# Performance work log

Hardware: AMD Instinct MI355X
Metric: run time of the kernel (lower is better)

## Reference

```python
import jax, jax.numpy as jnp
import numpy as np

GRID = 32
N_NODES = GRID * GRID          # 1024
PATCH = 1
C_IN = 3
NODE_F = C_IN * PATCH * PATCH  # 3
HID = 256
N_CLASSES = 10


def _build_norm_adj():
    # 5-point grid stencil + self loops, symmetrically normalized: D^-1/2 A D^-1/2
    adj = np.zeros((N_NODES, N_NODES), dtype=np.float32)
    idx = np.arange(N_NODES)
    i, j = idx // GRID, idx % GRID
    adj[idx, idx] = 1.0
    for di, dj in [(-1, 0), (1, 0), (0, -1), (0, 1)]:
        ni, nj = i + di, j + dj
        ok = (ni >= 0) & (ni < GRID) & (nj >= 0) & (nj < GRID)
        adj[idx[ok], (ni * GRID + nj)[ok]] = 1.0
    deg = adj.sum(axis=1)
    dis = np.where(deg > 0, deg ** -0.5, 0.0).astype(np.float32)
    return jnp.asarray(dis[:, None] * adj * dis[None, :])


def _image_to_graph(x):
    # [B,C,H,W] -> [B, grid, patch, grid, patch] blocks -> [B, N, C*patch^2]
    B = x.shape[0]
    x = x.reshape(B, C_IN, GRID, PATCH, GRID, PATCH)
    x = jnp.transpose(x, (0, 2, 4, 1, 3, 5))
    return x.reshape(B, N_NODES, NODE_F)


def setup_inputs() -> dict:
    key = jax.random.key(0)
    ks = jax.random.split(key, 10)
    s = 0.05
    return {
        "x": jax.random.normal(ks[0], (256, 3, 32, 32), dtype=jnp.float32),
        "W1": jax.random.normal(ks[1], (HID, NODE_F), dtype=jnp.float32) * s,
        "b1": jnp.zeros((HID,), dtype=jnp.float32),
        "W2": jax.random.normal(ks[2], (HID, HID), dtype=jnp.float32) * s,
        "b2": jnp.zeros((HID,), dtype=jnp.float32),
        "W3": jax.random.normal(ks[3], (HID // 2, HID), dtype=jnp.float32) * s,
        "b3": jnp.zeros((HID // 2,), dtype=jnp.float32),
        "Wc": jax.random.normal(ks[4], (N_CLASSES, N_NODES * (HID // 2)), dtype=jnp.float32) * s,
        "bc": jnp.zeros((N_CLASSES,), dtype=jnp.float32),
        "adj": _build_norm_adj(),
    }


def _gc(h, W, b, adj):
    # Linear, then fixed-adjacency aggregation, then ReLU
    h = jnp.einsum('bnf,hf->bnh', h, W) + b
    h = jnp.einsum('mn,bnh->bmh', adj, h)
    return jax.nn.relu(h)


def reference(x, W1, b1, W2, b2, W3, b3, Wc, bc, adj):
    h = _image_to_graph(x)                 # [B, N, 3]
    h = _gc(h, W1, b1, adj)                # [B, N, 256]
    h = _gc(h, W2, b2, adj)                # [B, N, 256]
    h = _gc(h, W3, b3, adj)                # [B, N, 128]
    h = h.reshape(h.shape[0], -1)          # [B, N*128]
    return h @ Wc.T + bc                   # [B, 10]
```

## Files before the change

kernel.cpp:

```cpp
#include <hip/hip_runtime.h>
#include <stdint.h>

#define N_NODES 1024
#define NCLS 10
#define KDIM 131072

typedef unsigned short u16;
typedef __bf16 bf16x8 __attribute__((ext_vector_type(8)));
typedef float f32x4 __attribute__((ext_vector_type(4)));

__device__ __forceinline__ float b2f(u16 u) {
  union { float f; uint32_t u; } v; v.u = ((uint32_t)u) << 16; return v.f;
}
__device__ __forceinline__ float b2f_lo(uint32_t u) {
  union { float f; uint32_t u; } v; v.u = u << 16; return v.f;
}
__device__ __forceinline__ float b2f_hi(uint32_t u) {
  union { float f; uint32_t u; } v; v.u = u & 0xFFFF0000u; return v.f;
}
__device__ __forceinline__ u16 f2b(float f) {
  union { float f; uint32_t u; } v; v.f = f;
  uint32_t r = v.u + 0x7FFF + ((v.u >> 16) & 1);
  return (u16)(r >> 16);
}
__device__ __forceinline__ uint32_t pack2(float a, float b) {
  return (uint32_t)f2b(a) | ((uint32_t)f2b(b) << 16);
}

__device__ __forceinline__ void async_copy16(const u16* g, u16* l) {
  __builtin_amdgcn_global_load_lds(
      (const __attribute__((address_space(1))) void*)g,
      (__attribute__((address_space(3))) void*)l, 16, 0, 0);
}

__global__ __launch_bounds__(256) void cvt_w_kernel(const float* __restrict__ w,
                                                    u16* __restrict__ o, int n) {
  int i = blockIdx.x * 256 + threadIdx.x;
  if (i < n) o[i] = f2b(w[i]);
}

__global__ __launch_bounds__(256) void prep_wc_kernel(const float* __restrict__ wc,
                                                      u16* __restrict__ o) {
  int i = blockIdx.x * 256 + threadIdx.x;
  int row = i >> 17;
  int col = i & (KDIM - 1);
  o[i] = (row < NCLS) ? f2b(wc[row * KDIM + col]) : (u16)0;
}

__global__ __launch_bounds__(256) void prep_tab_kernel(const float* __restrict__ adj,
                                                       int* __restrict__ nbi,
                                                       float* __restrict__ nbc,
                                                       float* __restrict__ r) {
  int m = blockIdx.x * 256 + threadIdx.x;
  if (m >= N_NODES) return;
  int i = m >> 5, j = m & 31;
  const float* arow = adj + (size_t)m * N_NODES;
  int n[5]; float c[5];
  n[0] = m;                      c[0] = arow[m];
  n[1] = (i > 0)  ? m - 32 : m;  c[1] = (i > 0)  ? arow[m - 32] : 0.f;
  n[2] = (i < 31) ? m + 32 : m;  c[2] = (i < 31) ? arow[m + 32] : 0.f;
  n[3] = (j > 0)  ? m - 1  : m;  c[3] = (j > 0)  ? arow[m - 1]  : 0.f;
  n[4] = (j < 31) ? m + 1  : m;  c[4] = (j < 31) ? arow[m + 1]  : 0.f;
  float s = 0.f;
#pragma unroll
  for (int t = 0; t < 5; t++) { nbi[m * 5 + t] = n[t]; nbc[m * 5 + t] = c[t]; s += c[t]; }
  r[m] = s;
}

__global__ __launch_bounds__(256) void outinit_kernel(const float* __restrict__ bc,
                                                      float* __restrict__ out) {
  int idx = blockIdx.x * 256 + threadIdx.x;
  if (idx < 256 * NCLS) out[idx] = bc[idx % NCLS];
}

__global__ __launch_bounds__(256) void l1agg_kernel(
    const float* __restrict__ x,
    const float* __restrict__ W1,
    const float* __restrict__ b1,
    const int* __restrict__ nbi, const float* __restrict__ nbc,
    const float* __restrict__ r,
    u16* __restrict__ g)
{
  __shared__ u16 h1s[128 * 256];
  __shared__ float gxs[128][4];
  __shared__ float W1s[768];
  __shared__ float b1s[256];
  int p0 = blockIdx.x * 64;
  int b = p0 >> 10;
  int m0 = p0 & 1023;
  int e0 = m0 - 32;
  int tid = threadIdx.x;

  b1s[tid] = b1[tid];
  for (int i = tid; i < 768; i += 256) W1s[i] = W1[i];

  if (tid < 128) {
    int n = e0 + tid;
    float g0 = 0.f, g1 = 0.f, g2 = 0.f, rn = 0.f;
    if (n >= 0 && n < N_NODES) {
      const float* xb = x + (size_t)b * 3072;
#pragma unroll
      for (int t = 0; t < 5; t++) {
        int nb = nbi[n * 5 + t]; float cf = nbc[n * 5 + t];
        g0 += cf * xb[nb];
        g1 += cf * xb[1024 + nb];
        g2 += cf * xb[2048 + nb];
      }
      rn = r[n];
    }
    gxs[tid][0] = g0; gxs[tid][1] = g1; gxs[tid][2] = g2; gxs[tid][3] = rn;
  }
  __syncthreads();

  int ch8 = (tid & 31) * 8;
  float w[8][3], bb[8];
#pragma unroll
  for (int c = 0; c < 8; c++) {
    w[c][0] = W1s[(ch8 + c) * 3];
    w[c][1] = W1s[(ch8 + c) * 3 + 1];
    w[c][2] = W1s[(ch8 + c) * 3 + 2];
    bb[c] = b1s[ch8 + c];
  }

#pragma unroll
  for (int it = 0; it < 16; it++) {
    int node = (tid >> 5) + it * 8;
    float g0 = gxs[node][0], g1 = gxs[node][1], g2 = gxs[node][2], rn = gxs[node][3];
    uint32_t pk[4];
#pragma unroll
    for (int c = 0; c < 8; c += 2) {
      float z0 = fmaxf(g0 * w[c][0] + g1 * w[c][1] + g2 * w[c][2] + rn * bb[c], 0.f);
      float z1 = fmaxf(g0 * w[c+1][0] + g1 * w[c+1][1] + g2 * w[c+1][2] + rn * bb[c+1], 0.f);
      pk[c >> 1] = pack2(z0, z1);
    }
    *(uint4*)&h1s[node * 256 + ch8] = *(uint4*)pk;
  }
  __syncthreads();

#pragma unroll
  for (int it = 0; it < 8; it++) {
    int node = (tid >> 5) + it * 8;
    int m = m0 + node;
    float acc[8] = {};
#pragma unroll
    for (int t = 0; t < 5; t++) {
      int nb = nbi[m * 5 + t]; float cf = nbc[m * 5 + t];
      uint4 v = *(const uint4*)&h1s[(nb - e0) * 256 + ch8];
      acc[0] += cf * b2f_lo(v.x); acc[1] += cf * b2f_hi(v.x);
      acc[2] += cf * b2f_lo(v.y); acc[3] += cf * b2f_hi(v.y);
      acc[4] += cf * b2f_lo(v.z); acc[5] += cf * b2f_hi(v.z);
      acc[6] += cf * b2f_lo(v.w); acc[7] += cf * b2f_hi(v.w);
    }
    uint4 o;
    o.x = pack2(acc[0], acc[1]); o.y = pack2(acc[2], acc[3]);
    o.z = pack2(acc[4], acc[5]); o.w = pack2(acc[6], acc[7]);
    *(uint4*)&g[(size_t)(p0 + node) * 256 + ch8] = o;
  }
}

__global__ __launch_bounds__(256) void agg_kernel(
    const u16* __restrict__ h,
    const int* __restrict__ nbi, const float* __restrict__ nbc,
    u16* __restrict__ g)
{
  int p = (blockIdx.x * 256 + threadIdx.x) >> 5;
  int lane = threadIdx.x & 31;
  int b = p >> 10, m = p & 1023;
  const u16* base = h + ((size_t)b << 10) * 256;
  int col = lane * 8;
  float acc[8] = {};
#pragma unroll
  for (int t = 0; t < 5; t++) {
    int nb = nbi[m * 5 + t]; float cf = nbc[m * 5 + t];
    uint4 v = *(const uint4*)(base + (size_t)nb * 256 + col);
    acc[0] += cf * b2f_lo(v.x); acc[1] += cf * b2f_hi(v.x);
    acc[2] += cf * b2f_lo(v.y); acc[3] += cf * b2f_hi(v.y);
    acc[4] += cf * b2f_lo(v.z); acc[5] += cf * b2f_hi(v.z);
    acc[6] += cf * b2f_lo(v.w); acc[7] += cf * b2f_hi(v.w);
  }
  uint4 o;
  o.x = pack2(acc[0], acc[1]); o.y = pack2(acc[2], acc[3]);
  o.z = pack2(acc[4], acc[5]); o.w = pack2(acc[6], acc[7]);
  *(uint4*)(g + (size_t)p * 256 + col) = o;
}

__global__ __launch_bounds__(256) void mm_kernel(
    const u16* __restrict__ A, const u16* __restrict__ W,
    const float* __restrict__ bias, const float* __restrict__ r,
    u16* __restrict__ C, int N)
{
  const int K = 256;
  __shared__ u16 As[128 * 32];
  __shared__ u16 Bs[128 * 32];
  int m0 = blockIdx.x * 128;
  int n0 = blockIdx.y * 128;
  int tid = threadIdx.x;
  int w = tid >> 6, l = tid & 63;
  int wm = w >> 1, wn = w & 1;

  f32x4 acc[4][4] = {};

  int srow = w * 32 + (l >> 2);
  int skoff = (l & 3) * 8;
  int lrow = l & 15, lq = l >> 4;

  for (int k0 = 0; k0 < K; k0 += 32) {
    const u16* ga = A + (size_t)(m0 + srow) * K + k0 + skoff;
    const u16* gb = W + (size_t)(n0 + srow) * K + k0 + skoff;
    async_copy16(ga,          &As[(w * 32) * 32]);
    async_copy16(ga + 16 * K, &As[(w * 32 + 16) * 32]);
    async_copy16(gb,          &Bs[(w * 32) * 32]);
    async_copy16(gb + 16 * K, &Bs[(w * 32 + 16) * 32]);
    __syncthreads();

    const u16* pa = &As[(wm * 64 + lrow) * 32 + lq * 8];
    const u16* pb = &Bs[(wn * 64 + lrow) * 32 + lq * 8];
    bf16x8 af[4], bf[4];
#pragma unroll
    for (int t = 0; t < 4; t++) {
      af[t] = *(const bf16x8*)(pa + t * 16 * 32);
      bf[t] = *(const bf16x8*)(pb + t * 16 * 32);
    }
#pragma unroll
    for (int mt = 0; mt < 4; mt++)
#pragma unroll
      for (int nt = 0; nt < 4; nt++)
        acc[mt][nt] = __builtin_amdgcn_mfma_f32_16x16x32_bf16(af[mt], bf[nt], acc[mt][nt], 0, 0, 0);
    __syncthreads();
  }

#pragma unroll
  for (int mt = 0; mt < 4; mt++)
#pragma unroll
    for (int nt = 0; nt < 4; nt++) {
      f32x4 v = acc[mt][nt];
      int col = n0 + wn * 64 + nt * 16 + lrow;
      float bs = bias[col];
#pragma unroll
      for (int i2 = 0; i2 < 4; i2++) {
        int row = m0 + wm * 64 + mt * 16 + lq * 4 + i2;
        float val = v[i2] + r[row & 1023] * bs;
        C[(size_t)row * N + col] = f2b(fmaxf(val, 0.f));
      }
    }
}

__global__ __launch_bounds__(256) void cls_kernel(
    const u16* __restrict__ h3,
    const u16* __restrict__ Wcb,
    float* __restrict__ out,
    int b0)
{
  int mt = blockIdx.x;
  int split = blockIdx.y;
  int w = threadIdx.x >> 6, l = threadIdx.x & 63;
  int lrow = l & 15, lq = l >> 4;
  f32x4 acc = {};
  int kbase = split * 4096 + w * 1024;
  const u16* pa = h3 + (size_t)(mt * 16 + lrow) * KDIM + kbase + lq * 8;
  const u16* pb = Wcb + (size_t)lrow * KDIM + kbase + lq * 8;
#pragma unroll 4
  for (int kk = 0; kk < 1024; kk += 32) {
    bf16x8 a = *(const bf16x8*)(pa + kk);
    bf16x8 b = *(const bf16x8*)(pb + kk);
    acc = __builtin_amdgcn_mfma_f32_16x16x32_bf16(a, b, acc, 0, 0, 0);
  }
  if (lrow < NCLS) {
#pragma unroll
    for (int i2 = 0; i2 < 4; i2++) {
      int b = b0 + mt * 16 + lq * 4 + i2;
      atomicAdd(&out[b * NCLS + lrow], acc[i2]);
    }
  }
}

extern "C" void kernel_launch(void* const* d_in, const int* in_sizes, int n_in,
                              void* d_out, int out_size, void* d_ws, size_t ws_size,
                              hipStream_t stream) {
  const float* x   = (const float*)d_in[0];
  const float* W1  = (const float*)d_in[1];
  const float* b1  = (const float*)d_in[2];
  const float* W2  = (const float*)d_in[3];
  const float* b2  = (const float*)d_in[4];
  const float* W3  = (const float*)d_in[5];
  const float* b3  = (const float*)d_in[6];
  const float* Wc  = (const float*)d_in[7];
  const float* bc  = (const float*)d_in[8];
  const float* adj = (const float*)d_in[9];
  float* out = (float*)d_out;
  const int B = 256;

  uint8_t* ws = (uint8_t*)d_ws;
  u16* W2b = (u16*)ws;  ws += (size_t)256 * 256 * 2;
  u16* W3b = (u16*)ws;  ws += (size_t)128 * 256 * 2;
  u16* Wcb = (u16*)ws;  ws += (size_t)16 * KDIM * 2;
  float* rr  = (float*)ws; ws += 1024 * 4;
  int*   nbi = (int*)ws;   ws += 1024 * 5 * 4;
  float* nbc = (float*)ws; ws += 1024 * 5 * 4;
  uintptr_t al = ((uintptr_t)ws + 255) & ~(uintptr_t)255;
  ws = (uint8_t*)al;
  size_t used = (size_t)(ws - (uint8_t*)d_ws);
  size_t avail = (ws_size > used) ? ws_size - used : 0;
  int chunk = 256;
  while (chunk > 32 && (size_t)chunk * 1024 * 256 * 2 * 2 > avail) chunk >>= 1;
  u16* bufA = (u16*)ws;
  u16* bufB = bufA + (size_t)chunk * 1024 * 256;

  cvt_w_kernel<<<256, 256, 0, stream>>>(W2, W2b, 256 * 256);
  cvt_w_kernel<<<128, 256, 0, stream>>>(W3, W3b, 128 * 256);
  prep_wc_kernel<<<(16 * KDIM) / 256, 256, 0, stream>>>(Wc, Wcb);
  prep_tab_kernel<<<4, 256, 0, stream>>>(adj, nbi, nbc, rr);
  outinit_kernel<<<(256 * NCLS + 255) / 256, 256, 0, stream>>>(bc, out);

  for (int b0 = 0; b0 < B; b0 += chunk) {
    const float* xb = x + (size_t)b0 * 3 * 1024;
    int M = chunk * 1024;
    l1agg_kernel<<<M / 64, 256, 0, stream>>>(xb, W1, b1, nbi, nbc, rr, bufB);
    {
      dim3 g(M / 128, 2);
      mm_kernel<<<g, 256, 0, stream>>>(bufB, W2b, b2, rr, bufA, 256);
    }
    agg_kernel<<<M / 8, 256, 0, stream>>>(bufA, nbi, nbc, bufB);
    {
      dim3 g(M / 128, 1);
      mm_kernel<<<g, 256, 0, stream>>>(bufB, W3b, b3, rr, bufA, 128);
    }
    dim3 gc(chunk / 16, 32);
    cls_kernel<<<gc, 256, 0, stream>>>(bufA, Wcb, out, b0);
  }
}
```

Measured before the change: 399.6 us.

## Fuse layer-3 aggregation into GEMM prologue and widen K tile with swizzled LDS

Removes the standalone aggregation kernel for layer 3. The 5-neighbor stencil sum is now computed while loading the A tile into LDS inside a new fused GEMM kernel, which avoids one full write and re-read of the intermediate activation buffer. The GEMM K step grows from 32 to 64 with an XOR-swizzled LDS layout to reduce bank conflicts and halve the number of barriers. The cost is that neighbor rows are gathered with plain synchronous loads in the GEMM prologue, and each block re-reads halo rows, which may stall the MFMA pipeline.

```diff
diff --git a/kernel.cpp b/kernel.cpp
--- a/kernel.cpp
+++ b/kernel.cpp
@@ -158,40 +158,14 @@
   }
 }
 
-__global__ __launch_bounds__(256) void agg_kernel(
-    const u16* __restrict__ h,
-    const int* __restrict__ nbi, const float* __restrict__ nbc,
-    u16* __restrict__ g)
-{
-  int p = (blockIdx.x * 256 + threadIdx.x) >> 5;
-  int lane = threadIdx.x & 31;
-  int b = p >> 10, m = p & 1023;
-  const u16* base = h + ((size_t)b << 10) * 256;
-  int col = lane * 8;
-  float acc[8] = {};
-#pragma unroll
-  for (int t = 0; t < 5; t++) {
-    int nb = nbi[m * 5 + t]; float cf = nbc[m * 5 + t];
-    uint4 v = *(const uint4*)(base + (size_t)nb * 256 + col);
-    acc[0] += cf * b2f_lo(v.x); acc[1] += cf * b2f_hi(v.x);
-    acc[2] += cf * b2f_lo(v.y); acc[3] += cf * b2f_hi(v.y);
-    acc[4] += cf * b2f_lo(v.z); acc[5] += cf * b2f_hi(v.z);
-    acc[6] += cf * b2f_lo(v.w); acc[7] += cf * b2f_hi(v.w);
-  }
-  uint4 o;
-  o.x = pack2(acc[0], acc[1]); o.y = pack2(acc[2], acc[3]);
-  o.z = pack2(acc[4], acc[5]); o.w = pack2(acc[6], acc[7]);
-  *(uint4*)(g + (size_t)p * 256 + col) = o;
-}
-
 __global__ __launch_bounds__(256) void mm_kernel(
     const u16* __restrict__ A, const u16* __restrict__ W,
     const float* __restrict__ bias, const float* __restrict__ r,
     u16* __restrict__ C, int N)
 {
   const int K = 256;
-  __shared__ u16 As[128 * 32];
-  __shared__ u16 Bs[128 * 32];
+  __shared__ u16 As[128 * 64];
+  __shared__ u16 Bs[128 * 64];
   int m0 = blockIdx.x * 128;
   int n0 = blockIdx.y * 128;
   int tid = threadIdx.x;
@@ -200,32 +174,40 @@
 
   f32x4 acc[4][4] = {};
 
-  int srow = w * 32 + (l >> 2);
-  int skoff = (l & 3) * 8;
+  int r8 = l >> 3, oct = l & 7;
+  int so = (oct ^ r8) << 3;
   int lrow = l & 15, lq = l >> 4;
-
-  for (int k0 = 0; k0 < K; k0 += 32) {
-    const u16* ga = A + (size_t)(m0 + srow) * K + k0 + skoff;
-    const u16* gb = W + (size_t)(n0 + srow) * K + k0 + skoff;
-    async_copy16(ga,          &As[(w * 32) * 32]);
-    async_copy16(ga + 16 * K, &As[(w * 32 + 16) * 32]);
-    async_copy16(gb,          &Bs[(w * 32) * 32]);
-    async_copy16(gb + 16 * K, &Bs[(w * 32 + 16) * 32]);
+  int o0 = (lq ^ (lrow & 7)) << 3;
+  int o1 = o0 ^ 32;
+
+  const u16* ga0 = A + (size_t)(m0 + w * 32 + r8) * K + so;
+  const u16* gb0 = W + (size_t)(n0 + w * 32 + r8) * K + so;
+
+  for (int k0 = 0; k0 < K; k0 += 64) {
+#pragma unroll
+    for (int q = 0; q < 4; q++) {
+      async_copy16(ga0 + q * 8 * K + k0, &As[(w * 32 + q * 8) * 64]);
+      async_copy16(gb0 + q * 8 * K + k0, &Bs[(w * 32 + q * 8) * 64]);
+    }
     __syncthreads();
 
-    const u16* pa = &As[(wm * 64 + lrow) * 32 + lq * 8];
-    const u16* pb = &Bs[(wn * 64 + lrow) * 32 + lq * 8];
-    bf16x8 af[4], bf[4];
+    const u16* pa = &As[(wm * 64 + lrow) * 64];
+    const u16* pb = &Bs[(wn * 64 + lrow) * 64];
+    bf16x8 af[4][2], bf[4][2];
 #pragma unroll
     for (int t = 0; t < 4; t++) {
-      af[t] = *(const bf16x8*)(pa + t * 16 * 32);
-      bf[t] = *(const bf16x8*)(pb + t * 16 * 32);
-    }
-#pragma unroll
-    for (int mt = 0; mt < 4; mt++)
-#pragma unroll
-      for (int nt = 0; nt < 4; nt++)
-        acc[mt][nt] = __builtin_amdgcn_mfma_f32_16x16x32_bf16(af[mt], bf[nt], acc[mt][nt], 0, 0, 0);
+      af[t][0] = *(const bf16x8*)(pa + t * 16 * 64 + o0);
+      af[t][1] = *(const bf16x8*)(pa + t * 16 * 64 + o1);
+      bf[t][0] = *(const bf16x8*)(pb + t * 16 * 64 + o0);
+      bf[t][1] = *(const bf16x8*)(pb + t * 16 * 64 + o1);
+    }
+#pragma unroll
+    for (int kh = 0; kh < 2; kh++)
+#pragma unroll
+      for (int mt = 0; mt < 4; mt++)
+#pragma unroll
+        for (int nt = 0; nt < 4; nt++)
+          acc[mt][nt] = __builtin_amdgcn_mfma_f32_16x16x32_bf16(af[mt][kh], bf[nt][kh], acc[mt][nt], 0, 0, 0);
     __syncthreads();
   }
 
@@ -235,6 +217,114 @@
     for (int nt = 0; nt < 4; nt++) {
       f32x4 v = acc[mt][nt];
       int col = n0 + wn * 64 + nt * 16 + lrow;
+      float bs = bias[col];
+#pragma unroll
+      for (int i2 = 0; i2 < 4; i2++) {
+        int row = m0 + wm * 64 + mt * 16 + lq * 4 + i2;
+        float val = v[i2] + r[row & 1023] * bs;
+        C[(size_t)row * N + col] = f2b(fmaxf(val, 0.f));
+      }
+    }
+}
+
+__global__ __launch_bounds__(256) void mm3agg_kernel(
+    const u16* __restrict__ H,
+    const u16* __restrict__ W,
+    const float* __restrict__ bias, const float* __restrict__ r,
+    const int* __restrict__ nbi, const float* __restrict__ nbc,
+    u16* __restrict__ C)
+{
+  const int K = 256, N = 128;
+  const int AST = 72;
+  __shared__ u16 As[128 * AST];
+  __shared__ u16 Bs[128 * 64];
+  int m0 = blockIdx.x * 128;
+  int tid = threadIdx.x;
+  int w = tid >> 6, l = tid & 63;
+  int wm = w >> 1, wn = w & 1;
+
+  f32x4 acc[4][4] = {};
+
+  int arow = tid >> 1;
+  int acol = (tid & 1) * 32;
+  int pg = m0 + arow;
+  int node = pg & 1023;
+  const u16* hb = H + ((size_t)(pg >> 10) << 10) * 256;
+  const u16* nbp[5]; float cf[5];
+#pragma unroll
+  for (int j = 0; j < 5; j++) {
+    nbp[j] = hb + (size_t)nbi[node * 5 + j] * 256 + acol;
+    cf[j] = nbc[node * 5 + j];
+  }
+
+  int r8 = l >> 3, oct = l & 7;
+  int so = (oct ^ r8) << 3;
+  const u16* gb0 = W + (size_t)(w * 32 + r8) * K + so;
+  int lrow = l & 15, lq = l >> 4;
+  int o0 = (lq ^ (lrow & 7)) << 3;
+  int o1 = o0 ^ 32;
+
+  for (int k0 = 0; k0 < K; k0 += 64) {
+#pragma unroll
+    for (int q = 0; q < 4; q++)
+      async_copy16(gb0 + q * 8 * K + k0, &Bs[(w * 32 + q * 8) * 64]);
+
+#pragma unroll
+    for (int half = 0; half < 2; half++) {
+      uint4 L[5][2];
+#pragma unroll
+      for (int j = 0; j < 5; j++) {
+        L[j][0] = *(const uint4*)(nbp[j] + k0 + half * 16);
+        L[j][1] = *(const uint4*)(nbp[j] + k0 + half * 16 + 8);
+      }
+      float a0[8] = {}, a1[8] = {};
+#pragma unroll
+      for (int j = 0; j < 5; j++) {
+        float c = cf[j];
+        const uint32_t* u0 = (const uint32_t*)&L[j][0];
+        const uint32_t* u1 = (const uint32_t*)&L[j][1];
+#pragma unroll
+        for (int e = 0; e < 4; e++) {
+          a0[2*e]   += c * b2f_lo(u0[e]); a0[2*e+1] += c * b2f_hi(u0[e]);
+          a1[2*e]   += c * b2f_lo(u1[e]); a1[2*e+1] += c * b2f_hi(u1[e]);
+        }
+      }
+      uint4 oa, ob;
+      oa.x = pack2(a0[0], a0[1]); oa.y = pack2(a0[2], a0[3]);
+      oa.z = pack2(a0[4], a0[5]); oa.w = pack2(a0[6], a0[7]);
+      ob.x = pack2(a1[0], a1[1]); ob.y = pack2(a1[2], a1[3]);
+      ob.z = pack2(a1[4], a1[5]); ob.w = pack2(a1[6], a1[7]);
+      *(uint4*)&As[arow * AST + acol + half * 16]     = oa;
+      *(uint4*)&As[arow * AST + acol + half * 16 + 8] = ob;
+    }
+    __syncthreads();
+
+    const u16* pa = &As[(wm * 64 + lrow) * AST];
+    const u16* pb = &Bs[(wn * 64 + lrow) * 64];
+    bf16x8 af[4][2], bf[4][2];
+#pragma unroll
+    for (int t = 0; t < 4; t++) {
+      af[t][0] = *(const bf16x8*)(pa + t * 16 * AST + lq * 8);
+      af[t][1] = *(const bf16x8*)(pa + t * 16 * AST + 32 + lq * 8);
+      bf[t][0] = *(const bf16x8*)(pb + t * 16 * 64 + o0);
+      bf[t][1] = *(const bf16x8*)(pb + t * 16 * 64 + o1);
+    }
+#pragma unroll
+    for (int kh = 0; kh < 2; kh++)
+#pragma unroll
+      for (int mt = 0; mt < 4; mt++)
+#pragma unroll
+        for (int nt = 0; nt < 4; nt++)
+          acc[mt][nt] = __builtin_amdgcn_mfma_f32_16x16x32_bf16(af[mt][kh], bf[nt][kh], acc[mt][nt], 0, 0, 0);
+    __syncthreads();
+  }
+
+#pragma unroll
+  for (int mt = 0; mt < 4; mt++)
+#pragma unroll
+    for (int nt = 0; nt < 4; nt++) {
+      f32x4 v = acc[mt][nt];
+      int col = wn * 64 + nt * 16 + lrow;
       float bs = bias[col];
 #pragma unroll
       for (int i2 = 0; i2 < 4; i2++) {
@@ -320,12 +410,8 @@
       dim3 g(M / 128, 2);
       mm_kernel<<<g, 256, 0, stream>>>(bufB, W2b, b2, rr, bufA, 256);
     }
-    agg_kernel<<<M / 8, 256, 0, stream>>>(bufA, nbi, nbc, bufB);
-    {
-      dim3 g(M / 128, 1);
-      mm_kernel<<<g, 256, 0, stream>>>(bufB, W3b, b3, rr, bufA, 128);
-    }
+    mm3agg_kernel<<<M / 128, 256, 0, stream>>>(bufA, W3b, b3, rr, nbi, nbc, bufB);
     dim3 gc(chunk / 16, 32);
-    cls_kernel<<<gc, 256, 0, stream>>>(bufA, Wcb, out, b0);
-  }
-}
+    cls_kernel<<<gc, 256, 0, stream>>>(bufB, Wcb, out, b0);
+  }
+}
```

Measured after the change: 378.8 us. -5.2%, faster.
